# Kernel tuning notes

Measured on AMD Instinct MI355X. Metric: run time of the kernel, lower is better.

Reference implementation:

```python
import jax, jax.numpy as jnp
import numpy as np


def _refl_conv(x, w, b, pad, stride):
    # ReflectionPad2d(pad) followed by Conv2d(stride=stride), NCHW / OIHW layouts.
    x = jnp.pad(x, ((0, 0), (0, 0), (pad, pad), (pad, pad)), mode='reflect')
    y = jax.lax.conv_general_dilated(
        x, w, window_strides=(stride, stride), padding='VALID',
        dimension_numbers=('NCHW', 'OIHW', 'NCHW'))
    return y + b[None, :, None, None]


def setup_inputs() -> dict:
    key = jax.random.key(0)
    ks = jax.random.split(key, 16)
    B, C, H, W = 8, 128, 64, 64
    IH, IW = 4 * H, 4 * W
    g = 0.02  # init gain ('normal' init in source)
    f32 = jnp.float32
    return {
        'feature_in': jax.random.normal(ks[0], (B, C, H, W), f32),
        'imgs': jax.random.uniform(ks[1], (B, 3, IH, IW), dtype=f32),
        'masks': jax.random.uniform(ks[2], (B, 1, IH, IW), dtype=f32),
        # Gate conv stack params (torch OIHW layout), biases zero per init_weights
        'gw1': g * jax.random.normal(ks[3], (32, 4, 7, 7), f32),
        'gb1': jnp.zeros((32,), f32),
        'gw2': g * jax.random.normal(ks[4], (64, 32, 5, 5), f32),
        'gb2': jnp.zeros((64,), f32),
        'gw3': g * jax.random.normal(ks[5], (128, 64, 5, 5), f32),
        'gb3': jnp.zeros((128,), f32),
        'gw4': g * jax.random.normal(ks[6], (256, 128, 3, 3), f32),
        'gb4': jnp.zeros((256,), f32),
        'gw5': g * jax.random.normal(ks[7], (1, 256, 3, 3), f32),
        'gb5': jnp.zeros((1,), f32),
        # combiner: Conv2d(2C -> C, 1x1)
        'cw': g * jax.random.normal(ks[8], (C, 2 * C, 1, 1), f32),
        'cb': jnp.zeros((C,), f32),
    }


def reference(feature_in, imgs, masks, gw1, gb1, gw2, gb2, gw3, gb3,
              gw4, gb4, gw5, gb5, cw, cb):
    PI = 3.1415926
    # ---- Gate ----
    x = jnp.concatenate([imgs, masks], axis=1)          # [B,4,4H,4W]
    s = jax.nn.relu(_refl_conv(x, gw1, gb1, 3, 1))
    s = jax.nn.relu(_refl_conv(s, gw2, gb2, 2, 2))
    s = jax.nn.relu(_refl_conv(s, gw3, gb3, 2, 1))
    s = jax.nn.relu(_refl_conv(s, gw4, gb4, 1, 2))
    s = jax.nn.relu(_refl_conv(s, gw5, gb5, 1, 1))      # [B,1,H,W]
    s = jnp.tan(PI * (jnp.tanh(s) - 0.5))
    B, C, H, W = feature_in.shape
    P = H * W
    gate = s.reshape(B, P, 1, 1)                        # row-major pixel order
    # ---- Att (patch_size=1: kernels are per-pixel feature vectors) ----
    K = feature_in.reshape(B, C, P).transpose(0, 2, 1) + 1e-7   # [B,P,C]
    Kn = K / jnp.sqrt(jnp.sum(K * K, axis=-1, keepdims=True))
    # attention_scores = conv2d(feature_map, K_norm) == cosine-like similarity
    scores = jnp.einsum('bpc,bcyx->bpyx', Kn, feature_in) + gate  # [B,P,H,W]
    A = jax.nn.softmax(scores, axis=1)
    # conv_transpose2d with 1x1 kernels == weighted sum of (unnormalized) kernels
    att = jnp.einsum('bpyx,bpc->bcyx', A, K)            # [B,C,H,W]
    # ---- combiner (1x1 conv on concat) ----
    cat = jnp.concatenate([att, feature_in], axis=1)    # [B,2C,H,W]
    out = jnp.einsum('oc,bcyx->boyx', cw[:, :, 0, 0], cat) + cb[None, :, None, None]
    return out
```

## Files before the change

kernel.cpp:

```cpp
#include <hip/hip_runtime.h>
#include <hip/hip_bf16.h>
#include <hip/hip_fp16.h>
#include <math.h>


#define PI_F 3.1415926f

typedef __attribute__((ext_vector_type(8))) short short8;
typedef __attribute__((ext_vector_type(4))) float f32x4;
typedef _Float16 half8 __attribute__((ext_vector_type(8)));
typedef __attribute__((ext_vector_type(4))) unsigned short u16x4;
typedef unsigned short ushort_t;

__device__ __forceinline__ ushort_t f2bf(float x) {
    unsigned u = __float_as_uint(x);
    unsigned r = (u + 0x7FFFu + ((u >> 16) & 1u)) >> 16;
    return (ushort_t)r;
}
__device__ __forceinline__ void split16(float x, ushort_t& h, ushort_t& l) {
    __half hh = __float2half(x);
    h = __half_as_ushort(hh);
    l = __half_as_ushort(__float2half(x - __half2float(hh)));
}
__device__ __forceinline__ ushort_t f2h(float x) {
    return __half_as_ushort(__float2half(x));
}
__device__ __forceinline__ int swz(int r, int c) {
    return ((c ^ r ^ (r >> 2)) & 3) << 3;
}

__global__ __launch_bounds__(256) void transform_w_k(
    const float* __restrict__ w, ushort_t* __restrict__ Wh, ushort_t* __restrict__ Wl,
    int Cout, int Cin, int KK)
{
    int idx = blockIdx.x * 256 + threadIdx.x;
    int N = Cout * Cin * KK;
    if (idx >= N) return;
    int oc = idx / (Cin * KK);
    int rem = idx - oc * (Cin * KK);
    int ic = rem / KK;
    int t = rem - ic * KK;
    float v = w[idx];
    long dst = ((long)t * Cout + oc) * Cin + ic;
    split16(v, Wh[dst], Wl[dst]);
}

__global__ __launch_bounds__(256) void transform_w1_k(
    const float* __restrict__ w, ushort_t* __restrict__ Wh, ushort_t* __restrict__ Wl)
{
    int idx = blockIdx.x * 256 + threadIdx.x;
    if (idx >= 7 * 32 * 32) return;
    int ky = idx / 1024;
    int rem = idx - ky * 1024;
    int oc = rem >> 5;
    int k = rem & 31;
    float v = 0.f;
    if (k < 28) {
        int kx = k >> 2, ic = k & 3;
        v = w[((oc * 4 + ic) * 7 + ky) * 7 + kx];
    }
    split16(v, Wh[idx], Wl[idx]);
}

__global__ __launch_bounds__(256) void prep_in_k(
    const float* __restrict__ imgs, const float* __restrict__ masks,
    ushort_t* __restrict__ Xh)
{
    const int iy = blockIdx.x, b = blockIdx.y;
    int sy = iy - 3; if (sy < 0) sy = -sy; if (sy >= 256) sy = 510 - sy;
    const int rb = sy << 8;
    const float* i0 = imgs + (long)b * 3 * 65536;
    const float* mk = masks + (long)b * 65536;
    for (int x = threadIdx.x; x < 262; x += 256) {
        int sx = x - 3; if (sx < 0) sx = -sx; if (sx >= 256) sx = 510 - sx;
        u16x4 hv;
        hv[0] = f2h(i0[rb + sx]);
        hv[1] = f2h(i0[65536 + rb + sx]);
        hv[2] = f2h(i0[131072 + rb + sx]);
        hv[3] = f2h(mk[rb + sx]);
        long o = ((long)(b * 262 + iy) * 262 + x) * 4;
        *(u16x4*)&Xh[o] = hv;
    }
}

__global__ __launch_bounds__(256) void conv1_mfma_k(
    const ushort_t* __restrict__ Xinh,
    const ushort_t* __restrict__ W1h, const ushort_t* __restrict__ W1l,
    const float* __restrict__ bias, ushort_t* __restrict__ Oh)
{
    const int tid = threadIdx.x, lane = tid & 63, wid = tid >> 6;
    const int wm = wid & 1, wn = wid >> 1, l15 = lane & 15, quad = lane >> 4;
    const int ox0 = blockIdx.x * 64;
    const int oy = blockIdx.y, b = blockIdx.z;
    f32x4 acc[2];
    acc[0] = (f32x4){0.f, 0.f, 0.f, 0.f};
    acc[1] = (f32x4){0.f, 0.f, 0.f, 0.f};
#pragma unroll
    for (int ky = 0; ky < 7; ++ky) {
        long wo = (long)(ky * 32 + wm * 16 + l15) * 32 + quad * 8;
        half8 Ah = *(const half8*)&W1h[wo];
        half8 Al = *(const half8*)&W1l[wo];
        long xrow = ((long)(b * 262 + oy + ky) * 262 + ox0) * 4;
#pragma unroll
        for (int ni = 0; ni < 2; ++ni) {
            long xo = xrow + (wn * 32 + ni * 16 + l15) * 4 + quad * 8;
            half8 Bh = *(const half8*)&Xinh[xo];
            acc[ni] = __builtin_amdgcn_mfma_f32_16x16x32_f16(Ah, Bh, acc[ni], 0, 0, 0);
            acc[ni] = __builtin_amdgcn_mfma_f32_16x16x32_f16(Al, Bh, acc[ni], 0, 0, 0);
        }
    }
    const int ocf = wm * 16 + quad * 4;
    float4 bv = *(const float4*)&bias[ocf];
#pragma unroll
    for (int ni = 0; ni < 2; ++ni) {
        int n = ox0 + wn * 32 + ni * 16 + l15;
        u16x4 hv;
        hv[0] = f2h(fmaxf(acc[ni][0] + bv.x, 0.f));
        hv[1] = f2h(fmaxf(acc[ni][1] + bv.y, 0.f));
        hv[2] = f2h(fmaxf(acc[ni][2] + bv.z, 0.f));
        hv[3] = f2h(fmaxf(acc[ni][3] + bv.w, 0.f));
        long o = ((long)(b * 260 + oy + 2) * 260 + n + 2) * 32 + ocf;
        *(u16x4*)&Oh[o] = hv;
    }
}

__global__ __launch_bounds__(256) void pad_cl_k(
    ushort_t* __restrict__ Xh, int Hp, int Wp, int PAD, int C, int H, int W)
{
    const int iy = blockIdx.x, b = blockIdx.y;
    int t = iy - PAD; if (t < 0) t = -t; if (t >= H) t = 2 * H - 2 - t;
    const int iys = t + PAD;
    const long rowd = ((long)(b * Hp + iy) * Wp) * C;
    const long rows = ((long)(b * Hp + iys) * Wp) * C;
    const int nch = Wp * (C >> 3);
    for (int idx = threadIdx.x; idx < nch; idx += 256) {
        int x = idx / (C >> 3);
        int cg = (idx - x * (C >> 3)) << 3;
        int t2 = x - PAD; if (t2 < 0) t2 = -t2; if (t2 >= W) t2 = 2 * W - 2 - t2;
        int xs = t2 + PAD;
        if (xs == x && iys == iy) continue;
        *(int4*)&Xh[rowd + (long)x * C + cg] = *(const int4*)&Xh[rows + (long)xs * C + cg];
    }
}

template<int K, int S, int CIN, int CSTG, int MT, int NPX, bool WRITE_CL>
__global__ __launch_bounds__(256, 2) void conv_mfma_k(
    const ushort_t* __restrict__ Xh,
    const ushort_t* __restrict__ Wh, const ushort_t* __restrict__ Wl,
    const float* __restrict__ bias,
    int Hp, int Wp, int CoutT,
    ushort_t* __restrict__ Oh, int Hpn, int Wpn, int NP,
    float* __restrict__ Ofp)
{
    constexpr int WS = (NPX - 1) * S + K;
    constexpr int WS2 = (WS + 1) / 2;
    constexpr int MF = MT / 32;
    constexpr int NF = NPX / 32;
    __shared__ ushort_t Bsh[WS * CSTG];
    __shared__ ushort_t Ash[K * MT * CSTG];
    __shared__ ushort_t Asl[K * MT * CSTG];
    const int tid = threadIdx.x, lane = tid & 63, wid = tid >> 6;
    const int wm = wid & 1, wn = wid >> 1, l15 = lane & 15, quad = lane >> 4;
    const int bx = blockIdx.x, oy = blockIdx.y;
    const int NOC = CoutT / MT;
    const int ocg = blockIdx.z % NOC, b = blockIdx.z / NOC;
    const int ox0 = bx * NPX;

    f32x4 acc[MF][NF];
#pragma unroll
    for (int mi = 0; mi < MF; ++mi)
#pragma unroll
        for (int ni = 0; ni < NF; ++ni) acc[mi][ni] = (f32x4){0.f, 0.f, 0.f, 0.f};

#pragma unroll
    for (int ky = 0; ky < K; ++ky) {
        const long rowoff = ((long)(b * Hp + oy * S + ky) * Wp + ox0 * S) * CIN;
        for (int cs = 0; cs < CIN; cs += CSTG) {
            __syncthreads();
            constexpr int NCH = WS * CSTG / 8;
#pragma unroll
            for (int it = 0; it < (NCH + 255) / 256; ++it) {
                int flat = tid + it * 256;
                if (flat < NCH) {
                    int e0 = flat * 8;
                    int x = e0 / CSTG;
                    int cpos = (e0 - x * CSTG) >> 3;
                    int xs = (S == 1) ? x : ((x >> 1) + (x & 1) * WS2);
                    *(int4*)&Bsh[xs * CSTG + swz(xs, cpos)] =
                        *(const int4*)&Xh[rowoff + (long)x * CIN + cs + cpos * 8];
                }
            }
            constexpr int NW = K * MT * CSTG / 8;
#pragma unroll
            for (int it = 0; it < (NW + 255) / 256; ++it) {
                int flat = tid + it * 256;
                if (flat < NW) {
                    int e0 = flat * 8;
                    int kx = e0 / (MT * CSTG);
                    int rem = e0 - kx * MT * CSTG;
                    int oc = rem / CSTG;
                    int cpos = (rem - oc * CSTG) >> 3;
                    int arow = kx * MT + oc;
                    int dst = arow * CSTG + swz(arow, cpos);
                    long src = ((long)((ky * K + kx) * CoutT + ocg * MT + oc)) * CIN + cs + cpos * 8;
                    *(int4*)&Ash[dst] = *(const int4*)&Wh[src];
                    *(int4*)&Asl[dst] = *(const int4*)&Wl[src];
                }
            }
            __syncthreads();
#pragma unroll
            for (int kx = 0; kx < K; ++kx) {
                half8 Ah[MF], Al[MF], Bh[NF];
#pragma unroll
                for (int mi = 0; mi < MF; ++mi) {
                    int arow = kx * MT + wm * (MT / 2) + mi * 16 + l15;
                    int ao = arow * CSTG + swz(arow, quad);
                    Ah[mi] = *(const half8*)&Ash[ao];
                    Al[mi] = *(const half8*)&Asl[ao];
                }
#pragma unroll
                for (int ni = 0; ni < NF; ++ni) {
                    int m = wn * (NPX / 2) + ni * 16 + l15;
                    int xs = (S == 1) ? (m + kx) : (m + (kx >> 1) + (kx & 1) * WS2);
                    Bh[ni] = *(const half8*)&Bsh[xs * CSTG + swz(xs, quad)];
                }
#pragma unroll
                for (int mi = 0; mi < MF; ++mi)
#pragma unroll
                    for (int ni = 0; ni < NF; ++ni) {
                        acc[mi][ni] = __builtin_amdgcn_mfma_f32_16x16x32_f16(Ah[mi], Bh[ni], acc[mi][ni], 0, 0, 0);
                        acc[mi][ni] = __builtin_amdgcn_mfma_f32_16x16x32_f16(Al[mi], Bh[ni], acc[mi][ni], 0, 0, 0);
                    }
            }
        }
    }
#pragma unroll
    for (int ni = 0; ni < NF; ++ni) {
        const int n = ox0 + wn * (NPX / 2) + ni * 16 + l15;
#pragma unroll
        for (int mi = 0; mi < MF; ++mi) {
            const int ocf = ocg * MT + wm * (MT / 2) + mi * 16 + quad * 4;
            float4 bv = *(const float4*)&bias[ocf];
            float v0 = fmaxf(acc[mi][ni][0] + bv.x, 0.f);
            float v1 = fmaxf(acc[mi][ni][1] + bv.y, 0.f);
            float v2 = fmaxf(acc[mi][ni][2] + bv.z, 0.f);
            float v3 = fmaxf(acc[mi][ni][3] + bv.w, 0.f);
            if (WRITE_CL) {
                long o = ((long)(b * Hpn + oy + NP) * Wpn + n + NP) * CoutT + ocf;
                u16x4 hv;
                hv[0] = f2h(v0); hv[1] = f2h(v1); hv[2] = f2h(v2); hv[3] = f2h(v3);
                *(u16x4*)&Oh[o] = hv;
            } else {
                long o = ((long)(b * CoutT + ocf) << 12) + (oy << 6) + n;
                Ofp[o] = v0;
                Ofp[o + 4096] = v1;
                Ofp[o + 8192] = v2;
                Ofp[o + 12288] = v3;
            }
        }
    }
}

__global__ __launch_bounds__(256, 2) void conv3_mfma_k(
    const ushort_t* __restrict__ Xh,
    const ushort_t* __restrict__ Wh, const ushort_t* __restrict__ Wl,
    const float* __restrict__ bias, ushort_t* __restrict__ Oh)
{
    __shared__ ushort_t Bsh[4][132 * 32];
    __shared__ ushort_t Ash[5 * 64 * 32];
    __shared__ ushort_t Asl[5 * 64 * 32];
    const int tid = threadIdx.x, lane = tid & 63, wid = tid >> 6;
    const int wm = wid & 1, wn = wid >> 1, l15 = lane & 15, quad = lane >> 4;
    const int oy0 = blockIdx.y * 4;
    const int ocg = blockIdx.z & 1, b = blockIdx.z >> 1;

    f32x4 acc[4][2][4];
#pragma unroll
    for (int oyi = 0; oyi < 4; ++oyi)
#pragma unroll
        for (int mi = 0; mi < 2; ++mi)
#pragma unroll
            for (int ni = 0; ni < 4; ++ni) acc[oyi][mi][ni] = (f32x4){0.f, 0.f, 0.f, 0.f};

    for (int csi = 0; csi < 2; ++csi) {
        const int cb = csi * 32;
        for (int flat = tid; flat < 3 * 528; flat += 256) {
            int r0 = flat / 528;
            int rem = flat - r0 * 528;
            int e0 = rem * 8;
            int x = e0 >> 5;
            int cpos = (e0 & 31) >> 3;
            *(int4*)&Bsh[r0][x * 32 + swz(x, cpos)] =
                *(const int4*)&Xh[((long)(b * 132 + oy0 + r0) * 132 + x) * 64 + cb + cpos * 8];
        }
        for (int ky = 0; ky < 5; ++ky) {
            {
                const int row = oy0 + ky + 3;
                const int slot = (ky + 3) & 3;
                for (int flat = tid; flat < 528; flat += 256) {
                    int e0 = flat * 8;
                    int x = e0 >> 5;
                    int cpos = (e0 & 31) >> 3;
                    *(int4*)&Bsh[slot][x * 32 + swz(x, cpos)] =
                        *(const int4*)&Xh[((long)(b * 132 + row) * 132 + x) * 64 + cb + cpos * 8];
                }
            }
            for (int flat = tid; flat < 1280; flat += 256) {
                int e0 = flat * 8;
                int kx = e0 >> 11;
                int rem = e0 & 2047;
                int oc = rem >> 5;
                int cpos = (rem & 31) >> 3;
                int arow = kx * 64 + oc;
                int dst = arow * 32 + swz(arow, cpos);
                long src = ((long)((ky * 5 + kx) * 128 + ocg * 64 + oc)) * 64 + cb + cpos * 8;
                *(int4*)&Ash[dst] = *(const int4*)&Wh[src];
                *(int4*)&Asl[dst] = *(const int4*)&Wl[src];
            }
            __syncthreads();
#pragma unroll
            for (int kx = 0; kx < 5; ++kx) {
                half8 Ah[2], Al[2];
#pragma unroll
                for (int mi = 0; mi < 2; ++mi) {
                    int arow = kx * 64 + wm * 32 + mi * 16 + l15;
                    int ao = arow * 32 + swz(arow, quad);
                    Ah[mi] = *(const half8*)&Ash[ao];
                    Al[mi] = *(const half8*)&Asl[ao];
                }
#pragma unroll
                for (int oyi = 0; oyi < 4; ++oyi) {
                    const int slot = (ky + oyi) & 3;
                    half8 Bh[4];
#pragma unroll
                    for (int ni = 0; ni < 4; ++ni) {
                        int xs = wn * 64 + ni * 16 + l15 + kx;
                        Bh[ni] = *(const half8*)&Bsh[slot][xs * 32 + swz(xs, quad)];
                    }
#pragma unroll
                    for (int mi = 0; mi < 2; ++mi)
#pragma unroll
                        for (int ni = 0; ni < 4; ++ni) {
                            acc[oyi][mi][ni] = __builtin_amdgcn_mfma_f32_16x16x32_f16(Ah[mi], Bh[ni], acc[oyi][mi][ni], 0, 0, 0);
                            acc[oyi][mi][ni] = __builtin_amdgcn_mfma_f32_16x16x32_f16(Al[mi], Bh[ni], acc[oyi][mi][ni], 0, 0, 0);
                        }
                }
            }
            __syncthreads();
        }
    }
    const int ocf = ocg * 64 + wm * 32 + quad * 4;
#pragma unroll
    for (int oyi = 0; oyi < 4; ++oyi) {
        const int oy = oy0 + oyi;
#pragma unroll
        for (int ni = 0; ni < 4; ++ni) {
            const int n = wn * 64 + ni * 16 + l15;
#pragma unroll
            for (int mi = 0; mi < 2; ++mi) {
                const int oc4 = ocf + mi * 16;
                float4 bv = *(const float4*)&bias[oc4];
                u16x4 hv;
                hv[0] = f2h(fmaxf(acc[oyi][mi][ni][0] + bv.x, 0.f));
                hv[1] = f2h(fmaxf(acc[oyi][mi][ni][1] + bv.y, 0.f));
                hv[2] = f2h(fmaxf(acc[oyi][mi][ni][2] + bv.z, 0.f));
                hv[3] = f2h(fmaxf(acc[oyi][mi][ni][3] + bv.w, 0.f));
                long o = ((long)(b * 130 + oy + 1) * 130 + n + 1) * 128 + oc4;
                *(u16x4*)&Oh[o] = hv;
            }
        }
    }
}

__global__ __launch_bounds__(256) void conv5_gate_k(
    const float* __restrict__ s4, const float* __restrict__ w,
    const float* __restrict__ bias, float* __restrict__ gate)
{
    const int tid = threadIdx.x;
    const int lane = tid & 63, g = tid >> 6;
    const int oy = blockIdx.x, b = blockIdx.y;
    int ixo[3], iyo[3];
#pragma unroll
    for (int k = 0; k < 3; ++k) {
        int ix = lane + k - 1; if (ix < 0) ix = -ix; if (ix >= 64) ix = 126 - ix;
        int iy = oy + k - 1; if (iy < 0) iy = -iy; if (iy >= 64) iy = 126 - iy;
        ixo[k] = ix; iyo[k] = iy << 6;
    }
    float part = 0.f;
    const float* inb = s4 + ((long)b * 256 + g * 64) * 4096;
    const float* wg = w + g * 64 * 9;
    for (int ic = 0; ic < 64; ++ic) {
        const float* inc = inb + ic * 4096;
        const float* wc = wg + ic * 9;
#pragma unroll
        for (int ky = 0; ky < 3; ++ky)
#pragma unroll
            for (int kx = 0; kx < 3; ++kx)
                part = fmaf(wc[ky * 3 + kx], inc[iyo[ky] + ixo[kx]], part);
    }
    __shared__ float red[4][64];
    red[g][lane] = part;
    __syncthreads();
    if (tid < 64) {
        float s = bias[0] + red[0][tid] + red[1][tid] + red[2][tid] + red[3][tid];
        s = fmaxf(s, 0.f);
        gate[(b << 12) + (oy << 6) + tid] = tanf(PI_F * (tanhf(s) - 0.5f));
    }
}

__global__ __launch_bounds__(256) void invn_k(const float* __restrict__ F, float* __restrict__ invn)
{
    const int p = blockIdx.x * 256 + threadIdx.x;
    const int b = blockIdx.y;
    const float* Fb = F + (long)b * 524288;
    float ss = 0.f;
#pragma unroll 8
    for (int c = 0; c < 128; ++c) {
        float v = Fb[c * 4096 + p] + 1e-7f;
        ss = fmaf(v, v, ss);
    }
    invn[(b << 12) + p] = 1.0f / sqrtf(ss);
}

__global__ __launch_bounds__(256) void prep_bf16_k(
    const float* __restrict__ F, ushort_t* __restrict__ Vf,
    ushort_t* __restrict__ Fa, ushort_t* __restrict__ Ft16)
{
    __shared__ float Ls[128][65];
    const int tid = threadIdx.x;
    const int lane = tid & 63, wv = tid >> 6;
    const int p0 = blockIdx.x * 64, b = blockIdx.y;
#pragma unroll 8
    for (int cc = 0; cc < 32; ++cc) {
        int c = wv * 32 + cc;
        long idx = ((long)b * 128 + c) * 4096 + p0 + lane;
        Ls[c][lane] = F[idx];
    }
    __syncthreads();
#pragma unroll 8
    for (int i = 0; i < 32; ++i) {
        int flat = tid + 256 * i;
        int c = flat & 127, pl_ = flat >> 7;
        Ft16[((long)b * 4096 + p0 + pl_) * 128 + c] = f2bf(Ls[c][pl_]);
    }
    const int chunk0 = blockIdx.x * 2;
#pragma unroll
    for (int s = tid; s < 1024; s += 256) {
        int ck = s >> 9, rem = s & 511;
        int ct = rem >> 6, ln = rem & 63;
        int c = ct * 16 + (ln & 15);
        int pl = ck * 32 + (ln >> 4) * 8;
        ushort_t tmp[8];
#pragma unroll
        for (int e = 0; e < 8; ++e) tmp[e] = f2bf(Ls[c][pl + e]);
        *(short8*)&Vf[(((long)(b * 128 + chunk0 + ck) * 8 + ct) * 64 + ln) * 8] = *(short8*)tmp;
    }
#pragma unroll
    for (int s = tid; s < 1024; s += 256) {
        int ck = s >> 9, rem = s & 511;
        int f = rem >> 6, ln = rem & 63;
        int l15_ = ln & 15;
        int c0 = (f & 3) * 32 + (ln >> 4) * 8;
        int pl = ck * 32 + ((l15_ & 12) << 1) + (l15_ & 3) + (f >> 2) * 4;
        ushort_t tmp[8];
#pragma unroll
        for (int e = 0; e < 8; ++e) tmp[e] = f2bf(Ls[c0 + e][pl]);
        *(short8*)&Fa[(((long)(b * 128 + chunk0 + ck) * 8 + f) * 64 + ln) * 8] = *(short8*)tmp;
    }
}

__global__ __launch_bounds__(64, 1) void flash_attn_k(
    const ushort_t* __restrict__ Ft16, const ushort_t* __restrict__ Vf,
    const ushort_t* __restrict__ Fa,
    const float* __restrict__ invn, const float* __restrict__ gate,
    float* __restrict__ Opart, float* __restrict__ lpart)
{
    const int lane = threadIdx.x & 63;
    const int l15 = lane & 15, quad = lane >> 4;
    const int b = blockIdx.x;
    const int qb = blockIdx.y & 63, ks = blockIdx.y >> 6;
    const int q0 = qb * 64;
    const int bp = b << 12;
    const ushort_t* Ftb = Ft16 + (long)b * 4096 * 128;
    const ushort_t* FaB = Fa + (long)b * 128 * 8 * 512;
    const ushort_t* VfB = Vf + (long)b * 128 * 8 * 512;

    short8 Bq[4][4];
#pragma unroll
    for (int ni = 0; ni < 4; ++ni)
#pragma unroll
        for (int cs = 0; cs < 4; ++cs)
            Bq[ni][cs] = *(const short8*)&Ftb[(long)(q0 + ni * 16 + l15) * 128 + cs * 32 + quad * 8];

    f32x4 O[8][4];
#pragma unroll
    for (int ct = 0; ct < 8; ++ct)
#pragma unroll
        for (int ni = 0; ni < 4; ++ni) O[ct][ni] = (f32x4){0.f, 0.f, 0.f, 0.f};
    float l_acc[4] = {0.f, 0.f, 0.f, 0.f};

    union BeU { short8 v; __hip_bfloat162 h[4]; };
    const int p_beg = ks * 1024;
    const int ck_beg = ks * 32;
    const long lane8 = (long)lane * 8;

    short8 Ap[2][2][4];
    short8 Va[2][8];
    float4 ivb[2][2], gtb[2][2];

    {
        const long fb = (long)(ck_beg) * 4096;
#pragma unroll
        for (int sub = 0; sub < 2; ++sub) {
#pragma unroll
            for (int cs = 0; cs < 4; ++cs)
                Ap[0][sub][cs] = *(const short8*)&FaB[fb + (long)(sub * 4 + cs) * 512 + lane8];
            ivb[0][sub] = *(const float4*)&invn[bp + p_beg + quad * 8 + sub * 4];
            gtb[0][sub] = *(const float4*)&gate[bp + p_beg + quad * 8 + sub * 4];
        }
#pragma unroll
        for (int ct = 0; ct < 8; ++ct)
            Va[0][ct] = *(const short8*)&VfB[fb + (long)ct * 512 + lane8];
    }

#pragma unroll 2
    for (int t = 0; t < 32; ++t) {
        const int cur = t & 1, nxt = cur ^ 1;
        if (t + 1 < 32) {
            const int p1 = p_beg + (t + 1) * 32;
            const long fb = (long)(ck_beg + t + 1) * 4096;
#pragma unroll
            for (int sub = 0; sub < 2; ++sub) {
#pragma unroll
                for (int cs = 0; cs < 4; ++cs)
                    Ap[nxt][sub][cs] = *(const short8*)&FaB[fb + (long)(sub * 4 + cs) * 512 + lane8];
                ivb[nxt][sub] = *(const float4*)&invn[bp + p1 + quad * 8 + sub * 4];
                gtb[nxt][sub] = *(const float4*)&gate[bp + p1 + quad * 8 + sub * 4];
            }
#pragma unroll
            for (int ct = 0; ct < 8; ++ct)
                Va[nxt][ct] = *(const short8*)&VfB[fb + (long)ct * 512 + lane8];
        }
        BeU be[4];
#pragma unroll
        for (int sub = 0; sub < 2; ++sub) {
            f32x4 Sa[4];
#pragma unroll
            for (int ni = 0; ni < 4; ++ni) Sa[ni] = (f32x4){0.f, 0.f, 0.f, 0.f};
#pragma unroll
            for (int cs = 0; cs < 4; ++cs)
#pragma unroll
                for (int ni = 0; ni < 4; ++ni)
                    Sa[ni] = __builtin_amdgcn_mfma_f32_16x16x32_bf16(Ap[cur][sub][cs], Bq[ni][cs], Sa[ni], 0, 0, 0);
            const float4 iv = ivb[cur][sub];
            const float4 gt = gtb[cur][sub];
#pragma unroll
            for (int ni = 0; ni < 4; ++ni) {
                float e0 = __expf(fmaf(Sa[ni][0], iv.x, gt.x));
                float e1 = __expf(fmaf(Sa[ni][1], iv.y, gt.y));
                float e2 = __expf(fmaf(Sa[ni][2], iv.z, gt.z));
                float e3 = __expf(fmaf(Sa[ni][3], iv.w, gt.w));
                be[ni].h[sub * 2]     = __float22bfloat162_rn(make_float2(e0, e1));
                be[ni].h[sub * 2 + 1] = __float22bfloat162_rn(make_float2(e2, e3));
                l_acc[ni] += (e0 + e1) + (e2 + e3);
            }
        }
#pragma unroll
        for (int ct = 0; ct < 8; ++ct)
#pragma unroll
            for (int ni = 0; ni < 4; ++ni)
                O[ct][ni] = __builtin_amdgcn_mfma_f32_16x16x32_bf16(Va[cur][ct], be[ni].v, O[ct][ni], 0, 0, 0);
    }

#pragma unroll
    for (int ni = 0; ni < 4; ++ni) {
        float lt = l_acc[ni];
        lt += __shfl_xor(lt, 16);
        lt += __shfl_xor(lt, 32);
        if (quad == 0)
            lpart[(ks * 8 + b) * 4096 + q0 + ni * 16 + l15] = lt;
    }
    float* Ob = Opart + (long)(ks * 8 + b) * 524288;
#pragma unroll
    for (int ct = 0; ct < 8; ++ct)
#pragma unroll
        for (int ni = 0; ni < 4; ++ni) {
            int c = ct * 16 + quad * 4;
            int q = q0 + ni * 16 + l15;
#pragma unroll
            for (int r = 0; r < 4; ++r)
                Ob[((long)(c + r) << 12) + q] = O[ct][ni][r];
        }
}

__global__ __launch_bounds__(256) void combiner_k(
    const float* __restrict__ Opart, const float* __restrict__ lpart,
    const float* __restrict__ F, const float* __restrict__ cw,
    const float* __restrict__ cb, float* __restrict__ out)
{
    const int tid = threadIdx.x;
    const int q = blockIdx.x * 256 + tid;
    const int o0 = blockIdx.y << 4;
    const int b = blockIdx.z;
    float lsum = 0.f;
#pragma unroll
    for (int ks = 0; ks < 4; ++ks) lsum += lpart[(ks * 8 + b) * 4096 + q];
    float il = 1.0f / lsum;
    const float* Fb = F + (long)b * 524288 + q;
    float acc[16];
#pragma unroll
    for (int j = 0; j < 16; ++j) acc[j] = cb[o0 + j];
    for (int c = 0; c < 128; ++c) {
        float a = 0.f;
#pragma unroll
        for (int ks = 0; ks < 4; ++ks)
            a += Opart[(long)(ks * 8 + b) * 524288 + (long)c * 4096 + q];
        a *= il;
        float f = Fb[(long)c * 4096];
#pragma unroll
        for (int j = 0; j < 16; ++j) {
            acc[j] = fmaf(cw[(o0 + j) * 256 + c], a, acc[j]);
            acc[j] = fmaf(cw[(o0 + j) * 256 + 128 + c], f, acc[j]);
        }
    }
#pragma unroll
    for (int j = 0; j < 16; ++j)
        out[((long)(b * 128 + o0 + j) << 12) + q] = acc[j];
}

extern "C" void kernel_launch(void* const* d_in, const int* in_sizes, int n_in,
                              void* d_out, int out_size, void* d_ws, size_t ws_size,
                              hipStream_t stream)
{
    const float* F     = (const float*)d_in[0];
    const float* imgs  = (const float*)d_in[1];
    const float* masks = (const float*)d_in[2];
    const float* gw1 = (const float*)d_in[3];  const float* gb1 = (const float*)d_in[4];
    const float* gw2 = (const float*)d_in[5];  const float* gb2 = (const float*)d_in[6];
    const float* gw3 = (const float*)d_in[7];  const float* gb3 = (const float*)d_in[8];
    const float* gw4 = (const float*)d_in[9];  const float* gb4 = (const float*)d_in[10];
    const float* gw5 = (const float*)d_in[11]; const float* gb5 = (const float*)d_in[12];
    const float* cw  = (const float*)d_in[13]; const float* cb  = (const float*)d_in[14];
    float* out = (float*)d_out;

    float* W = (float*)d_ws;
    ushort_t* Xcl2h = (ushort_t*)(W);
    ushort_t* Xcl4h = (ushort_t*)(W);
    float*    Opart = W;
    float*    lpart = W + 16777216;
    ushort_t* Xcl3h = (ushort_t*)(W + 17305600);
    ushort_t* Vf    = (ushort_t*)(W + 17305600);
    float*    s4   = W + 26226688;
    ushort_t* Fa   = (ushort_t*)(W + 26226688);
    ushort_t* Ft16 = (ushort_t*)(W + 30420992);
    ushort_t* W2h = (ushort_t*)(W + 34615296);
    ushort_t* W2l = (ushort_t*)(W + 34640896);
    ushort_t* W3h = (ushort_t*)(W + 34666496);
    ushort_t* W3l = (ushort_t*)(W + 34768896);
    ushort_t* W4h = (ushort_t*)(W + 34871296);
    ushort_t* W4l = (ushort_t*)(W + 35018752);
    float* gate = W + 35166208;
    float* invn = W + 35198976;
    ushort_t* Xinh = (ushort_t*)(W + 35231744);
    ushort_t* W1h  = (ushort_t*)(W + 37428416);
    ushort_t* W1l  = (ushort_t*)(W + 37432000);

    transform_w_k<<<dim3(200),  256, 0, stream>>>(gw2, W2h, W2l, 64, 32, 25);
    transform_w_k<<<dim3(800),  256, 0, stream>>>(gw3, W3h, W3l, 128, 64, 25);
    transform_w_k<<<dim3(1152), 256, 0, stream>>>(gw4, W4h, W4l, 256, 128, 9);
    transform_w1_k<<<dim3(28), 256, 0, stream>>>(gw1, W1h, W1l);
    prep_in_k<<<dim3(262, 8), 256, 0, stream>>>(imgs, masks, Xinh);

    conv1_mfma_k<<<dim3(4, 256, 8), 256, 0, stream>>>(Xinh, W1h, W1l, gb1, Xcl2h);
    pad_cl_k<<<dim3(260, 8), 256, 0, stream>>>(Xcl2h, 260, 260, 2, 32, 256, 256);
    conv_mfma_k<5, 2, 32, 32, 64, 128, true><<<dim3(1, 128, 8), 256, 0, stream>>>(
        Xcl2h, W2h, W2l, gb2, 260, 260, 64, Xcl3h, 132, 132, 2, nullptr);
    pad_cl_k<<<dim3(132, 8), 256, 0, stream>>>(Xcl3h, 132, 132, 2, 64, 128, 128);
    conv3_mfma_k<<<dim3(1, 32, 16), 256, 0, stream>>>(Xcl3h, W3h, W3l, gb3, Xcl4h);
    pad_cl_k<<<dim3(130, 8), 256, 0, stream>>>(Xcl4h, 130, 130, 1, 128, 128, 128);
    conv_mfma_k<3, 2, 128, 32, 128, 64, false><<<dim3(1, 64, 16), 256, 0, stream>>>(
        Xcl4h, W4h, W4l, gb4, 130, 130, 256, nullptr, 0, 0, 0, s4);
    conv5_gate_k<<<dim3(64, 8), 256, 0, stream>>>(s4, gw5, gb5, gate);

    invn_k<<<dim3(16, 8), 256, 0, stream>>>(F, invn);
    prep_bf16_k<<<dim3(64, 8), 256, 0, stream>>>(F, Vf, Fa, Ft16);
    flash_attn_k<<<dim3(8, 256, 1), 64, 0, stream>>>(Ft16, Vf, Fa, invn, gate, Opart, lpart);
    combiner_k<<<dim3(16, 8, 8), 256, 0, stream>>>(Opart, lpart, F, cw, cb, out);
}
```

Baseline: 561.9 us.

## Stage query fragments in LDS, drop register prefetch, allow two waves per SIMD

Measured after the change: 630.0 us. 1.12x slower.

```diff
diff --git a/kernel.cpp b/kernel.cpp
--- a/kernel.cpp
+++ b/kernel.cpp
@@ -424,7 +424,7 @@
 
 __global__ __launch_bounds__(256) void prep_bf16_k(
     const float* __restrict__ F, ushort_t* __restrict__ Vf,
-    ushort_t* __restrict__ Fa, ushort_t* __restrict__ Ft16)
+    ushort_t* __restrict__ Fa, ushort_t* __restrict__ Qf)
 {
     __shared__ float Ls[128][65];
     const int tid = threadIdx.x;
@@ -437,12 +437,6 @@
         Ls[c][lane] = F[idx];
     }
     __syncthreads();
-#pragma unroll 8
-    for (int i = 0; i < 32; ++i) {
-        int flat = tid + 256 * i;
-        int c = flat & 127, pl_ = flat >> 7;
-        Ft16[((long)b * 4096 + p0 + pl_) * 128 + c] = f2bf(Ls[c][pl_]);
-    }
     const int chunk0 = blockIdx.x * 2;
 #pragma unroll
     for (int s = tid; s < 1024; s += 256) {
@@ -467,30 +461,42 @@
         for (int e = 0; e < 8; ++e) tmp[e] = f2bf(Ls[c0 + e][pl]);
         *(short8*)&Fa[(((long)(b * 128 + chunk0 + ck) * 8 + f) * 64 + ln) * 8] = *(short8*)tmp;
     }
-}
-
-__global__ __launch_bounds__(64, 1) void flash_attn_k(
-    const ushort_t* __restrict__ Ft16, const ushort_t* __restrict__ Vf,
+#pragma unroll
+    for (int s = tid; s < 1024; s += 256) {
+        int f = s >> 6, ln = s & 63;
+        int ni = f >> 2, cs = f & 3;
+        int row = ni * 16 + (ln & 15);
+        int c0 = cs * 32 + (ln >> 4) * 8;
+        ushort_t tmp[8];
+#pragma unroll
+        for (int e = 0; e < 8; ++e) tmp[e] = f2bf(Ls[c0 + e][row]);
+        *(short8*)&Qf[(((long)(b * 64 + blockIdx.x) * 16 + f) * 64 + ln) * 8] = *(short8*)tmp;
+    }
+}
+
+__global__ __launch_bounds__(64, 2) void flash_attn_k(
+    const ushort_t* __restrict__ Qf, const ushort_t* __restrict__ Vf,
     const ushort_t* __restrict__ Fa,
     const float* __restrict__ invn, const float* __restrict__ gate,
     float* __restrict__ Opart, float* __restrict__ lpart)
 {
+    __shared__ ushort_t Qs[16 * 64 * 8];
     const int lane = threadIdx.x & 63;
     const int l15 = lane & 15, quad = lane >> 4;
     const int b = blockIdx.x;
     const int qb = blockIdx.y & 63, ks = blockIdx.y >> 6;
     const int q0 = qb * 64;
     const int bp = b << 12;
-    const ushort_t* Ftb = Ft16 + (long)b * 4096 * 128;
     const ushort_t* FaB = Fa + (long)b * 128 * 8 * 512;
     const ushort_t* VfB = Vf + (long)b * 128 * 8 * 512;
-
-    short8 Bq[4][4];
-#pragma unroll
-    for (int ni = 0; ni < 4; ++ni)
-#pragma unroll
-        for (int cs = 0; cs < 4; ++cs)
-            Bq[ni][cs] = *(const short8*)&Ftb[(long)(q0 + ni * 16 + l15) * 128 + cs * 32 + quad * 8];
+    const long lane8 = (long)lane * 8;
+
+    {
+        const ushort_t* QfB = Qf + ((long)(b * 64 + qb)) * 16 * 512;
+#pragma unroll
+        for (int f = 0; f < 16; ++f)
+            *(short8*)&Qs[(f * 64 + lane) * 8] = *(const short8*)&QfB[(long)f * 512 + lane8];
+    }
 
     f32x4 O[8][4];
 #pragma unroll
@@ -502,74 +508,59 @@
     union BeU { short8 v; __hip_bfloat162 h[4]; };
     const int p_beg = ks * 1024;
     const int ck_beg = ks * 32;
-    const long lane8 = (long)lane * 8;
-
-    short8 Ap[2][2][4];
-    short8 Va[2][8];
-    float4 ivb[2][2], gtb[2][2];
-
-    {
-        const long fb = (long)(ck_beg) * 4096;
+
+    for (int t = 0; t < 32; ++t) {
+        const int p0w = p_beg + t * 32;
+        const long fb = (long)(ck_beg + t) * 4096;
+        short8 Ap[2][4];
+#pragma unroll
+        for (int sub = 0; sub < 2; ++sub)
+#pragma unroll
+            for (int cs = 0; cs < 4; ++cs)
+                Ap[sub][cs] = *(const short8*)&FaB[fb + (long)(sub * 4 + cs) * 512 + lane8];
+        float4 iv[2], gt[2];
 #pragma unroll
         for (int sub = 0; sub < 2; ++sub) {
-#pragma unroll
-            for (int cs = 0; cs < 4; ++cs)
-                Ap[0][sub][cs] = *(const short8*)&FaB[fb + (long)(sub * 4 + cs) * 512 + lane8];
-            ivb[0][sub] = *(const float4*)&invn[bp + p_beg + quad * 8 + sub * 4];
-            gtb[0][sub] = *(const float4*)&gate[bp + p_beg + quad * 8 + sub * 4];
-        }
-#pragma unroll
-        for (int ct = 0; ct < 8; ++ct)
-            Va[0][ct] = *(const short8*)&VfB[fb + (long)ct * 512 + lane8];
-    }
-
-#pragma unroll 2
-    for (int t = 0; t < 32; ++t) {
-        const int cur = t & 1, nxt = cur ^ 1;
-        if (t + 1 < 32) {
-            const int p1 = p_beg + (t + 1) * 32;
-            const long fb = (long)(ck_beg + t + 1) * 4096;
-#pragma unroll
-            for (int sub = 0; sub < 2; ++sub) {
-#pragma unroll
-                for (int cs = 0; cs < 4; ++cs)
-                    Ap[nxt][sub][cs] = *(const short8*)&FaB[fb + (long)(sub * 4 + cs) * 512 + lane8];
-                ivb[nxt][sub] = *(const float4*)&invn[bp + p1 + quad * 8 + sub * 4];
-                gtb[nxt][sub] = *(const float4*)&gate[bp + p1 + quad * 8 + sub * 4];
-            }
-#pragma unroll
-            for (int ct = 0; ct < 8; ++ct)
-                Va[nxt][ct] = *(const short8*)&VfB[fb + (long)ct * 512 + lane8];
+            iv[sub] = *(const float4*)&invn[bp + p0w + quad * 8 + sub * 4];
+            gt[sub] = *(const float4*)&gate[bp + p0w + quad * 8 + sub * 4];
+        }
+        f32x4 Sa[2][4];
+#pragma unroll
+        for (int sub = 0; sub < 2; ++sub)
+#pragma unroll
+            for (int ni = 0; ni < 4; ++ni) Sa[sub][ni] = (f32x4){0.f, 0.f, 0.f, 0.f};
+#pragma unroll
+        for (int cs = 0; cs < 4; ++cs) {
+            short8 Bt[4];
+#pragma unroll
+            for (int ni = 0; ni < 4; ++ni)
+                Bt[ni] = *(const short8*)&Qs[((ni * 4 + cs) * 64 + lane) * 8];
+#pragma unroll
+            for (int sub = 0; sub < 2; ++sub)
+#pragma unroll
+                for (int ni = 0; ni < 4; ++ni)
+                    Sa[sub][ni] = __builtin_amdgcn_mfma_f32_16x16x32_bf16(Ap[sub][cs], Bt[ni], Sa[sub][ni], 0, 0, 0);
         }
         BeU be[4];
 #pragma unroll
-        for (int sub = 0; sub < 2; ++sub) {
-            f32x4 Sa[4];
-#pragma unroll
-            for (int ni = 0; ni < 4; ++ni) Sa[ni] = (f32x4){0.f, 0.f, 0.f, 0.f};
-#pragma unroll
-            for (int cs = 0; cs < 4; ++cs)
-#pragma unroll
-                for (int ni = 0; ni < 4; ++ni)
-                    Sa[ni] = __builtin_amdgcn_mfma_f32_16x16x32_bf16(Ap[cur][sub][cs], Bq[ni][cs], Sa[ni], 0, 0, 0);
-            const float4 iv = ivb[cur][sub];
-            const float4 gt = gtb[cur][sub];
+        for (int sub = 0; sub < 2; ++sub)
 #pragma unroll
             for (int ni = 0; ni < 4; ++ni) {
-                float e0 = __expf(fmaf(Sa[ni][0], iv.x, gt.x));
-                float e1 = __expf(fmaf(Sa[ni][1], iv.y, gt.y));
-                float e2 = __expf(fmaf(Sa[ni][2], iv.z, gt.z));
-                float e3 = __expf(fmaf(Sa[ni][3], iv.w, gt.w));
+                float e0 = __expf(fmaf(Sa[sub][ni][0], iv[sub].x, gt[sub].x));
+                float e1 = __expf(fmaf(Sa[sub][ni][1], iv[sub].y, gt[sub].y));
+                float e2 = __expf(fmaf(Sa[sub][ni][2], iv[sub].z, gt[sub].z));
+                float e3 = __expf(fmaf(Sa[sub][ni][3], iv[sub].w, gt[sub].w));
                 be[ni].h[sub * 2]     = __float22bfloat162_rn(make_float2(e0, e1));
                 be[ni].h[sub * 2 + 1] = __float22bfloat162_rn(make_float2(e2, e3));
                 l_acc[ni] += (e0 + e1) + (e2 + e3);
             }
-        }
-#pragma unroll
-        for (int ct = 0; ct < 8; ++ct)
+#pragma unroll
+        for (int ct = 0; ct < 8; ++ct) {
+            short8 Va = *(const short8*)&VfB[fb + (long)ct * 512 + lane8];
 #pragma unroll
             for (int ni = 0; ni < 4; ++ni)
-                O[ct][ni] = __builtin_amdgcn_mfma_f32_16x16x32_bf16(Va[cur][ct], be[ni].v, O[ct][ni], 0, 0, 0);
+                O[ct][ni] = __builtin_amdgcn_mfma_f32_16x16x32_bf16(Va, be[ni].v, O[ct][ni], 0, 0, 0);
+        }
     }
 
 #pragma unroll
@@ -650,9 +641,9 @@
     float*    lpart = W + 16777216;
     ushort_t* Xcl3h = (ushort_t*)(W + 17305600);
     ushort_t* Vf    = (ushort_t*)(W + 17305600);
+    ushort_t* Qf    = (ushort_t*)(W + 22000000);
     float*    s4   = W + 26226688;
     ushort_t* Fa   = (ushort_t*)(W + 26226688);
-    ushort_t* Ft16 = (ushort_t*)(W + 30420992);
     ushort_t* W2h = (ushort_t*)(W + 34615296);
     ushort_t* W2l = (ushort_t*)(W + 34640896);
     ushort_t* W3h = (ushort_t*)(W + 34666496);
@@ -683,7 +674,7 @@
     conv5_gate_k<<<dim3(64, 8), 256, 0, stream>>>(s4, gw5, gb5, gate);
 
     invn_k<<<dim3(16, 8), 256, 0, stream>>>(F, invn);
-    prep_bf16_k<<<dim3(64, 8), 256, 0, stream>>>(F, Vf, Fa, Ft16);
-    flash_attn_k<<<dim3(8, 256, 1), 64, 0, stream>>>(Ft16, Vf, Fa, invn, gate, Opart, lpart);
+    prep_bf16_k<<<dim3(64, 8), 256, 0, stream>>>(F, Vf, Fa, Qf);
+    flash_attn_k<<<dim3(8, 256, 1), 64, 0, stream>>>(Qf, Vf, Fa, invn, gate, Opart, lpart);
     combiner_k<<<dim3(16, 8, 8), 256, 0, stream>>>(Opart, lpart, F, cw, cb, out);
 }
```
